# Optimization experiments

Hardware: AMD Instinct MI355X
Metric: run time of the kernel (lower is better)

Reference implementation:

```python
import jax, jax.numpy as jnp
import numpy as np
import math

B, N, E, D = 4, 8192, 1024, 64

def setup_inputs() -> dict:
    key = jax.random.key(0)
    kx, kq, kk, kv, ko = jax.random.split(key, 5)
    x = jax.random.normal(kx, (B, N, E), dtype=jnp.float32)
    # ImplicitLinear weights: hash-generated Rademacher-like values scaled by 1/sqrt(in_features).
    # We stand in with sign(normal) * scale, matching the statistics of v_mask_generative * scale.
    wq = jnp.sign(jax.random.normal(kq, (D, E), dtype=jnp.float32)) / math.sqrt(E)
    wk = jnp.sign(jax.random.normal(kk, (D, E), dtype=jnp.float32)) / math.sqrt(E)
    wv = jnp.sign(jax.random.normal(kv, (D, E), dtype=jnp.float32)) / math.sqrt(E)
    wo = jnp.sign(jax.random.normal(ko, (E, D), dtype=jnp.float32)) / math.sqrt(D)
    return {"x": x, "wq": wq, "wk": wk, "wv": wv, "wo": wo}

def reference(x, wq, wk, wv, wo):
    # Projections: ImplicitLinear computes x @ W.T with W shaped [out, in]
    Q = jnp.einsum('bne,de->bnd', x, wq)   # [B,N,D]
    K = jnp.einsum('bne,de->bnd', x, wk)   # [B,N,D]
    V = jnp.einsum('bne,de->bnd', x, wv)   # [B,N,D]
    # ground mode: linear attention, energy = K^T @ V  -> [B,D,D]
    energy = jnp.einsum('bnd,bne->bde', K, V)
    context = jnp.einsum('bnd,bde->bne', Q, energy)  # [B,N,D]
    context = context * jnp.asarray(math.sqrt(3.0 / D), dtype=context.dtype)
    out = jnp.einsum('bnd,ed->bne', context, wo)  # [B,N,E]
    return out
```

## Files before the change

kernel.cpp:

```cpp
#include <hip/hip_runtime.h>
#include <hip/hip_bf16.h>
#include <stdint.h>


typedef __bf16 bf16x8 __attribute__((ext_vector_type(8)));
typedef __bf16 bf16x4 __attribute__((ext_vector_type(4)));
typedef float  f32x4  __attribute__((ext_vector_type(4)));

#define MFMA_BF16(A, Bb, C) __builtin_amdgcn_mfma_f32_16x16x32_bf16(A, Bb, C, 0, 0, 0)

__device__ __forceinline__ int swz8(int row, int slot) { return (slot ^ (row & 7)) << 3; }

__device__ __forceinline__ void gload_lds16(const void* g, void* l) {
    __builtin_amdgcn_global_load_lds(
        (const __attribute__((address_space(1))) unsigned int*)g,
        (__attribute__((address_space(3))) unsigned int*)l, 16, 0, 0);
}

__global__ __launch_bounds__(256) void prep_kernel(
    const float* __restrict__ wq, const float* __restrict__ wk,
    const float* __restrict__ wv, const float* __restrict__ wo,
    __bf16* __restrict__ Wt, __bf16* __restrict__ Wob)
{
    const int idx = blockIdx.x * 256 + threadIdx.x;
    if (idx < 24576) {
        const int col  = idx >> 7;
        const int rem  = idx & 127;
        const int step = rem >> 3;
        const int slot = rem & 7;
        const float* src = (col < 64)  ? wq + (size_t)col * 1024
                         : (col < 128) ? wk + (size_t)(col - 64) * 1024
                                       : wv + (size_t)(col - 128) * 1024;
        src += step * 64 + slot * 8;
        float w[8];
        *(float4*)&w[0] = *(const float4*)(src);
        *(float4*)&w[4] = *(const float4*)(src + 4);
        bf16x8 wb;
#pragma unroll
        for (int j = 0; j < 8; ++j) wb[j] = (__bf16)w[j];
        *(bf16x8*)&Wt[(size_t)step * 12288 + col * 64 + swz8(col, slot)] = wb;
    } else {
        const int c2 = idx - 24576;
        const int e  = c2 >> 3;
        const int s  = c2 & 7;
        float w[8];
        *(float4*)&w[0] = *(const float4*)&wo[(size_t)e * 64 + s * 8];
        *(float4*)&w[4] = *(const float4*)&wo[(size_t)e * 64 + s * 8 + 4];
        bf16x8 wb;
#pragma unroll
        for (int j = 0; j < 8; ++j) wb[j] = (__bf16)w[j];
        *(bf16x8*)&Wob[(size_t)e * 64 + s * 8] = wb;
    }
}

__global__ __launch_bounds__(512) void qkv_kernel(
    const float* __restrict__ x, const __bf16* __restrict__ Wt,
    __bf16* __restrict__ Qh, __bf16* __restrict__ Ql,
    float* __restrict__ Kf, float* __restrict__ Vf)
{
    __shared__ __bf16 xh[64 * 64];
    __shared__ __bf16 xl[64 * 64];
    __shared__ __bf16 wl[2][192 * 64];

    const int tid  = threadIdx.x;
    const int lane = tid & 63;
    const int wid  = tid >> 6;
    const int lr   = lane & 15;
    const int kg   = lane >> 4;
    const int wm   = wid >> 2;
    const int wn   = wid & 3;
    const int row0 = blockIdx.x * 64;

    f32x4 acc[2][3];
#pragma unroll
    for (int i = 0; i < 2; ++i)
#pragma unroll
        for (int j = 0; j < 3; ++j) acc[i][j] = (f32x4){0.f, 0.f, 0.f, 0.f};

    float xv[8];

#define STAGE_W(stp, buf)                                                      \
    {                                                                          \
        _Pragma("unroll")                                                      \
        for (int i = 0; i < 3; ++i) {                                          \
            const int boff = wid * 3072 + i * 1024;                            \
            gload_lds16((const char*)Wt + (size_t)(stp) * 24576 + boff + (lane << 4), \
                        (char*)&wl[buf][0] + boff);                            \
        }                                                                      \
    }
#define LOAD_X(stp)                                                            \
    {                                                                          \
        _Pragma("unroll")                                                      \
        for (int i = 0; i < 2; ++i) {                                          \
            const int s4 = tid + i * 512;                                      \
            const int r  = s4 >> 4, f4 = s4 & 15;                              \
            *(float4*)&xv[i * 4] =                                             \
                *(const float4*)&x[(size_t)(row0 + r) * 1024 + (stp) * 64 + f4 * 4]; \
        }                                                                      \
    }

    STAGE_W(0, 0);
    LOAD_X(0);

    for (int step = 0; step < 16; ++step) {
        const int cur = step & 1;
#pragma unroll
        for (int i = 0; i < 2; ++i) {
            const int s4 = tid + i * 512;
            const int r  = s4 >> 4, f4 = s4 & 15;
            bf16x4 h, l;
#pragma unroll
            for (int j = 0; j < 4; ++j) {
                const float v = xv[i * 4 + j];
                const unsigned int bb = __float_as_uint(v);
                h[j] = __builtin_bit_cast(__bf16, (unsigned short)(bb >> 16));
                l[j] = (__bf16)(v - __uint_as_float(bb & 0xffff0000u));
            }
            const int off = r * 64 + swz8(r, f4 >> 1) + (f4 & 1) * 4;
            *(bf16x4*)&xh[off] = h;
            *(bf16x4*)&xl[off] = l;
        }
        __syncthreads();
        if (step < 15) {
            STAGE_W(step + 1, cur ^ 1);
            LOAD_X(step + 1);
        }
#pragma unroll
        for (int ks = 0; ks < 2; ++ks) {
            const int slot = ks * 4 + kg;
            bf16x8 Ah[2], Al[2], Bw[3];
#pragma unroll
            for (int am = 0; am < 2; ++am) {
                const int row = wm * 32 + am * 16 + lr;
                Ah[am] = *(const bf16x8*)&xh[row * 64 + swz8(row, slot)];
                Al[am] = *(const bf16x8*)&xl[row * 64 + swz8(row, slot)];
            }
#pragma unroll
            for (int bn = 0; bn < 3; ++bn) {
                const int col = wn * 48 + bn * 16 + lr;
                Bw[bn] = *(const bf16x8*)&wl[cur][col * 64 + swz8(col, slot)];
            }
#pragma unroll
            for (int am = 0; am < 2; ++am)
#pragma unroll
                for (int bn = 0; bn < 3; ++bn) {
                    acc[am][bn] = MFMA_BF16(Ah[am], Bw[bn], acc[am][bn]);
                    acc[am][bn] = MFMA_BF16(Al[am], Bw[bn], acc[am][bn]);
                }
        }
        __syncthreads();
    }
#undef STAGE_W
#undef LOAD_X

#pragma unroll
    for (int am = 0; am < 2; ++am)
#pragma unroll
        for (int bn = 0; bn < 3; ++bn) {
            const int col  = wn * 48 + bn * 16 + lr;
            const int rowb = row0 + wm * 32 + am * 16 + kg * 4;
            if (col < 64) {
#pragma unroll
                for (int r = 0; r < 4; ++r) {
                    const int n   = rowb + r;
                    const float v = acc[am][bn][r];
                    const __bf16 h = (__bf16)v;
                    const __bf16 l = (__bf16)(v - (float)h);
                    const size_t o = (size_t)n * 64 + swz8(n, col >> 3) + (col & 7);
                    Qh[o] = h; Ql[o] = l;
                }
            } else if (col < 128) {
#pragma unroll
                for (int r = 0; r < 4; ++r)
                    Kf[(size_t)(rowb + r) * 64 + (col - 64)] = acc[am][bn][r];
            } else {
#pragma unroll
                for (int r = 0; r < 4; ++r)
                    Vf[(size_t)(rowb + r) * 64 + (col - 128)] = acc[am][bn][r];
            }
        }
}

__global__ __launch_bounds__(512) void energy_partial_kernel(
    const float* __restrict__ Kf, const float* __restrict__ Vf,
    float* __restrict__ part)
{
    __shared__ float lK[32 * 64];
    __shared__ float lV[32 * 64];
    const int tid  = threadIdx.x;
    const int lane = tid & 63;
    const int wid  = tid >> 6;
    const int d    = tid >> 3;
    const int e0   = (tid & 7) * 8;
    const int row0 = blockIdx.x * 128;

    float acc[8] = {0.f, 0.f, 0.f, 0.f, 0.f, 0.f, 0.f, 0.f};

    for (int c = 0; c < 4; ++c) {
        const size_t boff = (size_t)(row0 + c * 32) * 256 + wid * 1024 + (lane << 4);
        gload_lds16((const char*)Kf + boff, (char*)lK + wid * 1024);
        gload_lds16((const char*)Vf + boff, (char*)lV + wid * 1024);
        __syncthreads();
        for (int n = 0; n < 32; ++n) {
            const float kv = lK[n * 64 + d];
            const float4 a = *(const float4*)&lV[n * 64 + e0];
            const float4 b = *(const float4*)&lV[n * 64 + e0 + 4];
            acc[0] += kv * a.x; acc[1] += kv * a.y; acc[2] += kv * a.z; acc[3] += kv * a.w;
            acc[4] += kv * b.x; acc[5] += kv * b.y; acc[6] += kv * b.z; acc[7] += kv * b.w;
        }
        __syncthreads();
    }
    float* p = part + (size_t)blockIdx.x * 4096 + d * 64 + e0;
    *(float4*)&p[0] = make_float4(acc[0], acc[1], acc[2], acc[3]);
    *(float4*)&p[4] = make_float4(acc[4], acc[5], acc[6], acc[7]);
}

__global__ __launch_bounds__(256) void energy_reduce_kernel(
    const float* __restrict__ part, __bf16* __restrict__ Eth, __bf16* __restrict__ Etl)
{
    const int b    = blockIdx.x >> 4;
    const int elem = ((blockIdx.x & 15) << 8) + threadIdx.x;
    float s = 0.f;
#pragma unroll 8
    for (int c = 0; c < 64; ++c)
        s += part[(size_t)(b * 64 + c) * 4096 + elem];
    s *= 0.2165063509461097f;
    const int d = elem >> 6, e = elem & 63;
    const __bf16 h = (__bf16)s;
    const __bf16 l = (__bf16)(s - (float)h);
    const size_t o = (size_t)b * 4096 + e * 64 + swz8(e, d >> 3) + (d & 7);
    Eth[o] = h; Etl[o] = l;
}

__global__ __launch_bounds__(512) void out_kernel(
    const __bf16* __restrict__ Qh, const __bf16* __restrict__ Ql,
    const __bf16* __restrict__ Eth, const __bf16* __restrict__ Etl,
    const __bf16* __restrict__ Wob, float* __restrict__ out)
{
    __shared__ __bf16 qh[64 * 64];
    __shared__ __bf16 ql[64 * 64];
    __shared__ __bf16 ch[64 * 64];
    __shared__ __bf16 cl[64 * 64];

    const int tid  = threadIdx.x;
    const int lane = tid & 63;
    const int wid  = tid >> 6;
    const int lr   = lane & 15;
    const int kg   = lane >> 4;
    const int wm   = wid >> 2;
    const int wn   = wid & 3;
    const int row0 = blockIdx.x * 64;
    const int b    = blockIdx.x >> 7;

    gload_lds16((const char*)Qh + (size_t)row0 * 128 + wid * 1024 + (lane << 4),
                (char*)qh + wid * 1024);
    gload_lds16((const char*)Ql + (size_t)row0 * 128 + wid * 1024 + (lane << 4),
                (char*)ql + wid * 1024);
    __syncthreads();

    f32x4 cacc[2];
    cacc[0] = (f32x4){0.f, 0.f, 0.f, 0.f};
    cacc[1] = (f32x4){0.f, 0.f, 0.f, 0.f};
#pragma unroll
    for (int ks = 0; ks < 2; ++ks) {
        const int slot = ks * 4 + kg;
        const int e    = wn * 16 + lr;
        const bf16x8 Bh = *(const bf16x8*)&Eth[(size_t)b * 4096 + e * 64 + swz8(e, slot)];
        const bf16x8 Bl = *(const bf16x8*)&Etl[(size_t)b * 4096 + e * 64 + swz8(e, slot)];
#pragma unroll
        for (int am = 0; am < 2; ++am) {
            const int row = wm * 32 + am * 16 + lr;
            const bf16x8 Ah = *(const bf16x8*)&qh[row * 64 + swz8(row, slot)];
            const bf16x8 Al = *(const bf16x8*)&ql[row * 64 + swz8(row, slot)];
            cacc[am] = MFMA_BF16(Ah, Bh, cacc[am]);
            cacc[am] = MFMA_BF16(Ah, Bl, cacc[am]);
            cacc[am] = MFMA_BF16(Al, Bh, cacc[am]);
        }
    }
#pragma unroll
    for (int am = 0; am < 2; ++am)
#pragma unroll
        for (int r = 0; r < 4; ++r) {
            const int n = wm * 32 + am * 16 + kg * 4 + r;
            const int dd = wn * 16 + lr;
            const float v  = cacc[am][r];
            const __bf16 h = (__bf16)v;
            const __bf16 l = (__bf16)(v - (float)h);
            const int off = n * 64 + swz8(n, dd >> 3) + (dd & 7);
            ch[off] = h; cl[off] = l;
        }
    __syncthreads();

    bf16x8 Ah[2][2], Al[2][2];
#pragma unroll
    for (int am = 0; am < 2; ++am)
#pragma unroll
        for (int ks = 0; ks < 2; ++ks) {
            const int row  = wm * 32 + am * 16 + lr;
            const int slot = ks * 4 + kg;
            Ah[am][ks] = *(const bf16x8*)&ch[row * 64 + swz8(row, slot)];
            Al[am][ks] = *(const bf16x8*)&cl[row * 64 + swz8(row, slot)];
        }
#pragma unroll
    for (int g = 0; g < 4; ++g) {
        f32x4 oacc[2][4];
#pragma unroll
        for (int i = 0; i < 2; ++i)
#pragma unroll
            for (int j = 0; j < 4; ++j) oacc[i][j] = (f32x4){0.f, 0.f, 0.f, 0.f};
#pragma unroll
        for (int ks = 0; ks < 2; ++ks) {
            bf16x8 Bw[4];
#pragma unroll
            for (int bn = 0; bn < 4; ++bn) {
                const int col = wn * 256 + g * 64 + bn * 16 + lr;
                Bw[bn] = *(const bf16x8*)&Wob[(size_t)col * 64 + ks * 32 + kg * 8];
            }
#pragma unroll
            for (int am = 0; am < 2; ++am)
#pragma unroll
                for (int bn = 0; bn < 4; ++bn) {
                    oacc[am][bn] = MFMA_BF16(Ah[am][ks], Bw[bn], oacc[am][bn]);
                    oacc[am][bn] = MFMA_BF16(Al[am][ks], Bw[bn], oacc[am][bn]);
                }
        }
#pragma unroll
        for (int am = 0; am < 2; ++am)
#pragma unroll
            for (int bn = 0; bn < 4; ++bn) {
                const int gcol = wn * 256 + g * 64 + bn * 16 + lr;
                const int grow = row0 + wm * 32 + am * 16 + kg * 4;
#pragma unroll
                for (int r = 0; r < 4; ++r)
                    __builtin_nontemporal_store(oacc[am][bn][r],
                        &out[(size_t)(grow + r) * 1024 + gcol]);
            }
    }
}

extern "C" void kernel_launch(void* const* d_in, const int* in_sizes, int n_in,
                              void* d_out, int out_size, void* d_ws, size_t ws_size,
                              hipStream_t stream)
{
    const float* x  = (const float*)d_in[0];
    const float* wq = (const float*)d_in[1];
    const float* wk = (const float*)d_in[2];
    const float* wv = (const float*)d_in[3];
    const float* wo = (const float*)d_in[4];
    float* out = (float*)d_out;

    char* ws = (char*)d_ws;
    __bf16* Qh   = (__bf16*)(ws);
    __bf16* Ql   = (__bf16*)(ws + 4194304);
    float*  Kf   = (float*)(ws + 8388608);
    float*  Vf   = (float*)(ws + 16777216);
    float*  part = (float*)(ws + 25165824);
    __bf16* Wt   = (__bf16*)(ws + 25165824);
    __bf16* Eth  = (__bf16*)(ws + 29360128);
    __bf16* Etl  = (__bf16*)(ws + 29392896);
    __bf16* Wob  = (__bf16*)(ws + 29425664);

    prep_kernel<<<128, 256, 0, stream>>>(wq, wk, wv, wo, Wt, Wob);
    qkv_kernel<<<512, 512, 0, stream>>>(x, Wt, Qh, Ql, Kf, Vf);
    energy_partial_kernel<<<256, 512, 0, stream>>>(Kf, Vf, part);
    energy_reduce_kernel<<<64, 256, 0, stream>>>(part, Eth, Etl);
    out_kernel<<<512, 512, 0, stream>>>(Qh, Ql, Eth, Etl, Wob, out);
}
```

Measured before the change: 293.5 us.

## Read QKV weights directly from global memory and store Q as fp32

The QKV projection kernel no longer stages weight tiles through LDS. Each wave now loads its B fragments straight from a plainly laid-out bf16 weight copy, which is small enough to stay cached. Blocks shrink to 32 rows and 4 waves, and the x tile is double-buffered so one barrier per step is dropped. Q is written as fp32 and split into hi/lo bf16 inside the output kernel, which simplifies the prep kernel's layout at the cost of more Q traffic and uncoalesced global weight reads.

```diff
diff --git a/kernel.cpp b/kernel.cpp
--- a/kernel.cpp
+++ b/kernel.cpp
@@ -4,7 +4,6 @@
 
 
 typedef __bf16 bf16x8 __attribute__((ext_vector_type(8)));
-typedef __bf16 bf16x4 __attribute__((ext_vector_type(4)));
 typedef float  f32x4  __attribute__((ext_vector_type(4)));
 
 #define MFMA_BF16(A, Bb, C) __builtin_amdgcn_mfma_f32_16x16x32_bf16(A, Bb, C, 0, 0, 0)
@@ -17,59 +16,42 @@
         (__attribute__((address_space(3))) unsigned int*)l, 16, 0, 0);
 }
 
-__global__ __launch_bounds__(256) void prep_kernel(
+__global__ __launch_bounds__(128) void prep_kernel(
     const float* __restrict__ wq, const float* __restrict__ wk,
     const float* __restrict__ wv, const float* __restrict__ wo,
-    __bf16* __restrict__ Wt, __bf16* __restrict__ Wob)
-{
-    const int idx = blockIdx.x * 256 + threadIdx.x;
-    if (idx < 24576) {
-        const int col  = idx >> 7;
-        const int rem  = idx & 127;
-        const int step = rem >> 3;
-        const int slot = rem & 7;
-        const float* src = (col < 64)  ? wq + (size_t)col * 1024
-                         : (col < 128) ? wk + (size_t)(col - 64) * 1024
-                                       : wv + (size_t)(col - 128) * 1024;
-        src += step * 64 + slot * 8;
-        float w[8];
-        *(float4*)&w[0] = *(const float4*)(src);
-        *(float4*)&w[4] = *(const float4*)(src + 4);
-        bf16x8 wb;
-#pragma unroll
-        for (int j = 0; j < 8; ++j) wb[j] = (__bf16)w[j];
-        *(bf16x8*)&Wt[(size_t)step * 12288 + col * 64 + swz8(col, slot)] = wb;
-    } else {
-        const int c2 = idx - 24576;
-        const int e  = c2 >> 3;
-        const int s  = c2 & 7;
-        float w[8];
-        *(float4*)&w[0] = *(const float4*)&wo[(size_t)e * 64 + s * 8];
-        *(float4*)&w[4] = *(const float4*)&wo[(size_t)e * 64 + s * 8 + 4];
-        bf16x8 wb;
-#pragma unroll
-        for (int j = 0; j < 8; ++j) wb[j] = (__bf16)w[j];
-        *(bf16x8*)&Wob[(size_t)e * 64 + s * 8] = wb;
-    }
-}
-
-__global__ __launch_bounds__(512) void qkv_kernel(
-    const float* __restrict__ x, const __bf16* __restrict__ Wt,
-    __bf16* __restrict__ Qh, __bf16* __restrict__ Ql,
-    float* __restrict__ Kf, float* __restrict__ Vf)
-{
-    __shared__ __bf16 xh[64 * 64];
-    __shared__ __bf16 xl[64 * 64];
-    __shared__ __bf16 wl[2][192 * 64];
+    __bf16* __restrict__ Wb)
+{
+    const int gid = blockIdx.x * 128 + threadIdx.x;
+    const int e0  = gid * 8;
+    const float* src = (e0 < 65536)  ? wq + e0
+                     : (e0 < 131072) ? wk + (e0 - 65536)
+                     : (e0 < 196608) ? wv + (e0 - 131072)
+                                     : wo + (e0 - 196608);
+    float w[8];
+    *(float4*)&w[0] = *(const float4*)(src);
+    *(float4*)&w[4] = *(const float4*)(src + 4);
+    bf16x8 wb;
+#pragma unroll
+    for (int j = 0; j < 8; ++j) wb[j] = (__bf16)w[j];
+    *(bf16x8*)&Wb[e0] = wb;
+}
+
+__global__ __launch_bounds__(256) void qkv_kernel(
+    const float* __restrict__ x, const __bf16* __restrict__ Wb,
+    float* __restrict__ Qf, float* __restrict__ Kf, float* __restrict__ Vf)
+{
+    __shared__ __bf16 xh[2][32 * 64];
+    __shared__ __bf16 xl[2][32 * 64];
 
     const int tid  = threadIdx.x;
     const int lane = tid & 63;
     const int wid  = tid >> 6;
     const int lr   = lane & 15;
     const int kg   = lane >> 4;
-    const int wm   = wid >> 2;
-    const int wn   = wid & 3;
-    const int row0 = blockIdx.x * 64;
+    const int row0 = blockIdx.x * 32;
+
+    const int sr = tid >> 3;
+    const int f8 = tid & 7;
 
     f32x4 acc[2][3];
 #pragma unroll
@@ -77,68 +59,50 @@
 #pragma unroll
         for (int j = 0; j < 3; ++j) acc[i][j] = (f32x4){0.f, 0.f, 0.f, 0.f};
 
-    float xv[8];
-
-#define STAGE_W(stp, buf)                                                      \
-    {                                                                          \
-        _Pragma("unroll")                                                      \
-        for (int i = 0; i < 3; ++i) {                                          \
-            const int boff = wid * 3072 + i * 1024;                            \
-            gload_lds16((const char*)Wt + (size_t)(stp) * 24576 + boff + (lane << 4), \
-                        (char*)&wl[buf][0] + boff);                            \
-        }                                                                      \
-    }
-#define LOAD_X(stp)                                                            \
-    {                                                                          \
-        _Pragma("unroll")                                                      \
-        for (int i = 0; i < 2; ++i) {                                          \
-            const int s4 = tid + i * 512;                                      \
-            const int r  = s4 >> 4, f4 = s4 & 15;                              \
-            *(float4*)&xv[i * 4] =                                             \
-                *(const float4*)&x[(size_t)(row0 + r) * 1024 + (stp) * 64 + f4 * 4]; \
-        }                                                                      \
-    }
-
-    STAGE_W(0, 0);
-    LOAD_X(0);
-
+    float xv[8], xn[8];
+
+#define LOAD_X(dst, stp)                                                        \
+    {                                                                           \
+        const float* src_ = &x[(size_t)(row0 + sr) * 1024 + (stp) * 64 + f8 * 8]; \
+        *(float4*)&dst[0] = *(const float4*)(src_);                             \
+        *(float4*)&dst[4] = *(const float4*)(src_ + 4);                         \
+    }
+
+    LOAD_X(xv, 0);
+
+#pragma unroll 2
     for (int step = 0; step < 16; ++step) {
         const int cur = step & 1;
-#pragma unroll
-        for (int i = 0; i < 2; ++i) {
-            const int s4 = tid + i * 512;
-            const int r  = s4 >> 4, f4 = s4 & 15;
-            bf16x4 h, l;
-#pragma unroll
-            for (int j = 0; j < 4; ++j) {
-                const float v = xv[i * 4 + j];
+        {
+            bf16x8 h, l;
+#pragma unroll
+            for (int j = 0; j < 8; ++j) {
+                const float v = xv[j];
                 const unsigned int bb = __float_as_uint(v);
                 h[j] = __builtin_bit_cast(__bf16, (unsigned short)(bb >> 16));
                 l[j] = (__bf16)(v - __uint_as_float(bb & 0xffff0000u));
             }
-            const int off = r * 64 + swz8(r, f4 >> 1) + (f4 & 1) * 4;
-            *(bf16x4*)&xh[off] = h;
-            *(bf16x4*)&xl[off] = l;
+            const int off = sr * 64 + swz8(sr, f8);
+            *(bf16x8*)&xh[cur][off] = h;
+            *(bf16x8*)&xl[cur][off] = l;
         }
         __syncthreads();
-        if (step < 15) {
-            STAGE_W(step + 1, cur ^ 1);
-            LOAD_X(step + 1);
-        }
+        if (step < 15) LOAD_X(xn, step + 1);
+
 #pragma unroll
         for (int ks = 0; ks < 2; ++ks) {
             const int slot = ks * 4 + kg;
             bf16x8 Ah[2], Al[2], Bw[3];
 #pragma unroll
             for (int am = 0; am < 2; ++am) {
-                const int row = wm * 32 + am * 16 + lr;
-                Ah[am] = *(const bf16x8*)&xh[row * 64 + swz8(row, slot)];
-                Al[am] = *(const bf16x8*)&xl[row * 64 + swz8(row, slot)];
+                const int row = am * 16 + lr;
+                Ah[am] = *(const bf16x8*)&xh[cur][row * 64 + swz8(row, slot)];
+                Al[am] = *(const bf16x8*)&xl[cur][row * 64 + swz8(row, slot)];
             }
 #pragma unroll
             for (int bn = 0; bn < 3; ++bn) {
-                const int col = wn * 48 + bn * 16 + lr;
-                Bw[bn] = *(const bf16x8*)&wl[cur][col * 64 + swz8(col, slot)];
+                const int col = wid * 48 + bn * 16 + lr;
+                Bw[bn] = *(const bf16x8*)&Wb[(size_t)col * 1024 + step * 64 + slot * 8];
             }
 #pragma unroll
             for (int am = 0; am < 2; ++am)
@@ -148,36 +112,22 @@
                     acc[am][bn] = MFMA_BF16(Al[am], Bw[bn], acc[am][bn]);
                 }
         }
-        __syncthreads();
-    }
-#undef STAGE_W
+#pragma unroll
+        for (int j = 0; j < 8; ++j) xv[j] = xn[j];
+    }
 #undef LOAD_X
 
 #pragma unroll
     for (int am = 0; am < 2; ++am)
 #pragma unroll
         for (int bn = 0; bn < 3; ++bn) {
-            const int col  = wn * 48 + bn * 16 + lr;
-            const int rowb = row0 + wm * 32 + am * 16 + kg * 4;
-            if (col < 64) {
-#pragma unroll
-                for (int r = 0; r < 4; ++r) {
-                    const int n   = rowb + r;
-                    const float v = acc[am][bn][r];
-                    const __bf16 h = (__bf16)v;
-                    const __bf16 l = (__bf16)(v - (float)h);
-                    const size_t o = (size_t)n * 64 + swz8(n, col >> 3) + (col & 7);
-                    Qh[o] = h; Ql[o] = l;
-                }
-            } else if (col < 128) {
-#pragma unroll
-                for (int r = 0; r < 4; ++r)
-                    Kf[(size_t)(rowb + r) * 64 + (col - 64)] = acc[am][bn][r];
-            } else {
-#pragma unroll
-                for (int r = 0; r < 4; ++r)
-                    Vf[(size_t)(rowb + r) * 64 + (col - 128)] = acc[am][bn][r];
-            }
+            const int col  = wid * 48 + bn * 16 + lr;
+            const int rowb = row0 + am * 16 + kg * 4;
+            float* dst = (col < 64) ? Qf : (col < 128) ? Kf : Vf;
+            const int cc = col & 63;
+#pragma unroll
+            for (int r = 0; r < 4; ++r)
+                dst[(size_t)(rowb + r) * 64 + cc] = acc[am][bn][r];
         }
 }
 
@@ -233,7 +183,7 @@
 }
 
 __global__ __launch_bounds__(512) void out_kernel(
-    const __bf16* __restrict__ Qh, const __bf16* __restrict__ Ql,
+    const float* __restrict__ Qf,
     const __bf16* __restrict__ Eth, const __bf16* __restrict__ Etl,
     const __bf16* __restrict__ Wob, float* __restrict__ out)
 {
@@ -252,10 +202,24 @@
     const int row0 = blockIdx.x * 64;
     const int b    = blockIdx.x >> 7;
 
-    gload_lds16((const char*)Qh + (size_t)row0 * 128 + wid * 1024 + (lane << 4),
-                (char*)qh + wid * 1024);
-    gload_lds16((const char*)Ql + (size_t)row0 * 128 + wid * 1024 + (lane << 4),
-                (char*)ql + wid * 1024);
+    {
+        const int r  = tid >> 3;
+        const int f8 = tid & 7;
+        const float* src = &Qf[(size_t)(row0 + r) * 64 + f8 * 8];
+        float v[8];
+        *(float4*)&v[0] = *(const float4*)(src);
+        *(float4*)&v[4] = *(const float4*)(src + 4);
+        bf16x8 h, l;
+#pragma unroll
+        for (int j = 0; j < 8; ++j) {
+            const unsigned int bb = __float_as_uint(v[j]);
+            h[j] = __builtin_bit_cast(__bf16, (unsigned short)(bb >> 16));
+            l[j] = (__bf16)(v[j] - __uint_as_float(bb & 0xffff0000u));
+        }
+        const int off = r * 64 + swz8(r, f8);
+        *(bf16x8*)&qh[off] = h;
+        *(bf16x8*)&ql[off] = l;
+    }
     __syncthreads();
 
     f32x4 cacc[2];
@@ -281,7 +245,7 @@
     for (int am = 0; am < 2; ++am)
 #pragma unroll
         for (int r = 0; r < 4; ++r) {
-            const int n = wm * 32 + am * 16 + kg * 4 + r;
+            const int n  = wm * 32 + am * 16 + kg * 4 + r;
             const int dd = wn * 16 + lr;
             const float v  = cacc[am][r];
             const __bf16 h = (__bf16)v;
@@ -350,19 +314,18 @@
     float* out = (float*)d_out;
 
     char* ws = (char*)d_ws;
-    __bf16* Qh   = (__bf16*)(ws);
-    __bf16* Ql   = (__bf16*)(ws + 4194304);
+    float*  Qf   = (float*)(ws);
     float*  Kf   = (float*)(ws + 8388608);
     float*  Vf   = (float*)(ws + 16777216);
     float*  part = (float*)(ws + 25165824);
-    __bf16* Wt   = (__bf16*)(ws + 25165824);
-    __bf16* Eth  = (__bf16*)(ws + 29360128);
-    __bf16* Etl  = (__bf16*)(ws + 29392896);
-    __bf16* Wob  = (__bf16*)(ws + 29425664);
-
-    prep_kernel<<<128, 256, 0, stream>>>(wq, wk, wv, wo, Wt, Wob);
-    qkv_kernel<<<512, 512, 0, stream>>>(x, Wt, Qh, Ql, Kf, Vf);
+    __bf16* Wb   = (__bf16*)(ws + 29360128);
+    __bf16* Wob  = (__bf16*)(ws + 29753344);
+    __bf16* Eth  = (__bf16*)(ws + 30408704);
+    __bf16* Etl  = (__bf16*)(ws + 30441472);
+
+    prep_kernel<<<256, 128, 0, stream>>>(wq, wk, wv, wo, Wb);
+    qkv_kernel<<<1024, 256, 0, stream>>>(x, Wb, Qf, Kf, Vf);
     energy_partial_kernel<<<256, 512, 0, stream>>>(Kf, Vf, part);
     energy_reduce_kernel<<<64, 256, 0, stream>>>(part, Eth, Etl);
-    out_kernel<<<512, 512, 0, stream>>>(Qh, Ql, Eth, Etl, Wob, out);
-}
+    out_kernel<<<512, 512, 0, stream>>>(Qf, Eth, Etl, Wob, out);
+}
```

New measurement: 309.0 us. +5.3%, slower.
